# Kernel tuning notes

Measured on AMD Instinct MI355X. Metric: run time of the kernel, lower is better.

The kernel has to match this reference:

```python
import jax, jax.numpy as jnp
import numpy as np

IMG = 840.0
MIN_SIZES = [[16.0, 32.0], [64.0, 128.0], [256.0, 512.0]]
STEPS = [8, 16, 32]
THRESH = 0.35      # neg_overlap / matching threshold used by this repo's MultiBoxLoss
NEG_POS = 7
LOC_WEIGHT = 2.0
VAR0, VAR1 = 0.1, 0.2


def _make_priors():
    out = []
    for ms, step in zip(MIN_SIZES, STEPS):
        f = int(np.ceil(IMG / step))
        jj, ii = np.meshgrid(np.arange(f), np.arange(f))  # j: cols (x), i: rows (y)
        cx = (jj + 0.5) * step / IMG
        cy = (ii + 0.5) * step / IMG
        for m in ms:
            s = np.full_like(cx, m / IMG)
            out.append(np.stack([cx, cy, s, s], axis=-1).reshape(-1, 4))
    return np.concatenate(out, axis=0).astype(np.float32)  # [29126, 4] (cx, cy, w, h)


def setup_inputs() -> dict:
    key = jax.random.key(0)
    k1, k2, k3, k4 = jax.random.split(key, 4)
    B, G = 64, 24
    priors = jnp.asarray(_make_priors())            # [P, 4]
    P = priors.shape[0]
    loc_data = 0.1 * jax.random.normal(k1, (B, P, 4), dtype=jnp.float32)
    conf_data = jax.random.normal(k2, (B, P, 2), dtype=jnp.float32)
    cxy = jax.random.uniform(k3, (B, G, 2), minval=0.2, maxval=0.8)
    wh = jax.random.uniform(k4, (B, G, 2), minval=0.05, maxval=0.3)
    gt_boxes = jnp.clip(jnp.concatenate([cxy - wh / 2, cxy + wh / 2], axis=-1), 1e-3, 1.0)
    gt_labels = jnp.ones((B, G), dtype=jnp.int32)   # single foreground class (num_classes=2)
    return {"loc_data": loc_data, "conf_data": conf_data, "gt_boxes": gt_boxes,
            "gt_labels": gt_labels, "priors": priors}


def _multibox_loss(loc_data, conf_data, gt_boxes, gt_labels, priors):
    B, P, _ = loc_data.shape
    G = gt_boxes.shape[1]
    # priors in point form for IoU
    pr_pt = jnp.concatenate([priors[:, :2] - priors[:, 2:] / 2,
                             priors[:, :2] + priors[:, 2:] / 2], axis=1)  # [P,4]
    area_p = (pr_pt[:, 2] - pr_pt[:, 0]) * (pr_pt[:, 3] - pr_pt[:, 1])

    def match_one(truths, labels):
        # IoU [G, P]
        lt = jnp.maximum(truths[:, None, :2], pr_pt[None, :, :2])
        rb = jnp.minimum(truths[:, None, 2:], pr_pt[None, :, 2:])
        wh = jnp.clip(rb - lt, 0.0)
        inter = wh[..., 0] * wh[..., 1]
        area_t = (truths[:, 2] - truths[:, 0]) * (truths[:, 3] - truths[:, 1])
        iou = inter / (area_t[:, None] + area_p[None, :] - inter)
        best_prior_idx = jnp.argmax(iou, axis=1)          # [G]
        bto = jnp.max(iou, axis=0)                        # [P] best truth overlap
        bti = jnp.argmax(iou, axis=0)                     # [P] best truth idx
        bto = bto.at[best_prior_idx].set(2.0)             # ensure each gt keeps its best prior
        bti = bti.at[best_prior_idx].set(jnp.arange(G))
        matched = truths[bti]                             # [P,4]
        conf = jnp.where(bto < THRESH, 0, labels[bti])    # [P]
        # encode (SSD style, variances 0.1/0.2)
        g_cxcy = ((matched[:, :2] + matched[:, 2:]) / 2 - priors[:, :2]) / (VAR0 * priors[:, 2:])
        g_wh = jnp.log((matched[:, 2:] - matched[:, :2]) / priors[:, 2:]) / VAR1
        return jnp.concatenate([g_cxcy, g_wh], axis=1), conf

    loc_t, conf_t = jax.vmap(match_one)(gt_boxes, gt_labels)  # [B,P,4], [B,P]
    pos = conf_t > 0                                          # [B,P]

    # localization: smooth L1 over positives
    diff = jnp.abs(loc_data - loc_t)
    sl1 = jnp.where(diff < 1.0, 0.5 * diff * diff, diff - 0.5)
    loss_l = jnp.sum(sl1 * pos[..., None].astype(loc_data.dtype))

    # per-prior CE = logsumexp - logit[target]
    lse = jax.nn.logsumexp(conf_data, axis=-1)                               # [B,P]
    gold = jnp.take_along_axis(conf_data, conf_t[..., None], axis=-1)[..., 0]
    ce_all = lse - gold                                                      # [B,P]

    # hard negative mining: rank background-class loss of negatives
    mine = jnp.where(pos, 0.0, ce_all)
    rank = jnp.argsort(jnp.argsort(-mine, axis=1), axis=1)
    num_pos = jnp.sum(pos, axis=1, keepdims=True)                            # [B,1]
    num_neg = jnp.minimum(NEG_POS * num_pos, P - 1)
    neg = rank < num_neg

    mask = pos | neg
    loss_c = jnp.sum(jnp.where(mask, ce_all, 0.0))

    N = jnp.maximum(jnp.sum(pos).astype(loc_data.dtype), 1.0)
    return loss_l / N, loss_c / N


def reference(loc_data, conf_data, gt_boxes, gt_labels, priors):
    loss_l, loss_c = _multibox_loss(loc_data, conf_data, gt_boxes, gt_labels, priors)
    return LOC_WEIGHT * loss_l + loss_c
```

## Files before the change

### kernel.cpp

```cpp
#include <hip/hip_runtime.h>

static constexpr int B_ = 64;
static constexpr int P_ = 29126;
static constexpr int G_ = 24;
static constexpr float THRESH_ = 0.35f;
static constexpr int NEGPOS_ = 7;
static constexpr int PBL_ = (P_ + 1023) / 1024;
static constexpr int PPAD_ = PBL_ * 1024;
static constexpr int NBL_ = PBL_ * B_;
static constexpr int WPB_ = 912;
static constexpr int CCS_ = 32;

__device__ const float LAD_[16] = {
    0.5f,    0.5901f, 0.6964f, 0.8220f, 0.9701f, 1.1450f, 1.3514f, 1.5950f,
    1.8825f, 2.2218f, 2.6223f, 3.0950f, 3.6529f, 4.3113f, 5.0885f, 6.0057f };

static constexpr size_t ZBYTES_ =
    (size_t)B_*WPB_*4 + (size_t)B_*CCS_*4 + 16;
static constexpr int ZVEC_ = (int)((ZBYTES_ + 15) / 16);

__global__ __launch_bounds__(256) void k_zero(ulonglong2* __restrict__ dst)
{
    const int i = blockIdx.x*256 + threadIdx.x;
    if (i < ZVEC_) dst[i] = make_ulonglong2(0ull, 0ull);
}

__global__ __launch_bounds__(256) void k_sparse(
    const float4* __restrict__ gt4,
    const float4* __restrict__ priors4,
    unsigned* __restrict__ matchw,
    unsigned long long* __restrict__ bp_pack)
{
    const int g = blockIdx.x;
    const int b = blockIdx.y;
    const int bg = b*G_ + g;
    const int tid = threadIdx.x;

    const float4 t = gt4[bg];
    const float area_t = (t.z - t.x) * (t.w - t.y);

    float bv = -1.0f; int bq = 0;

#pragma unroll
    for (int r = 0; r < 6; ++r) {
        const int   f    = (r < 2) ? 105 : (r < 4) ? 53 : 27;
        const float sc   = (r < 2) ? 105.0f : (r < 4) ? 52.5f : 26.25f;
        const int   base = (r == 0) ? 0 : (r == 1) ? 11025 : (r == 2) ? 22050
                         : (r == 3) ? 24859 : (r == 4) ? 27668 : 28397;
        const float hw   = ((r == 0) ? 16.0f : (r == 1) ? 32.0f : (r == 2) ? 64.0f
                         : (r == 3) ? 128.0f : (r == 4) ? 256.0f : 512.0f)
                           * (0.5f / 840.0f);

        const int j0 = max(0,     (int)floorf((t.x - hw)*sc - 0.5f) - 1);
        const int j1 = min(f - 1, (int)ceilf ((t.z + hw)*sc - 0.5f) + 1);
        const int i0 = max(0,     (int)floorf((t.y - hw)*sc - 0.5f) - 1);
        const int i1 = min(f - 1, (int)ceilf ((t.w + hw)*sc - 0.5f) + 1);
        const int W = j1 - j0 + 1;
        const int n = W * (i1 - i0 + 1);

        for (int c = tid; c < n; c += 256) {
            const int ii = c / W;
            const int jj = c - ii*W;
            const int p = base + (i0 + ii)*f + (j0 + jj);
            const float4 pr = priors4[p];
            const float hx = pr.z * 0.5f, hy = pr.w * 0.5f;
            const float px0 = pr.x - hx, py0 = pr.y - hy;
            const float px1 = pr.x + hx, py1 = pr.y + hy;
            const float area_p = (px1 - px0) * (py1 - py0);
            const float lx = fmaxf(t.x, px0), ly = fmaxf(t.y, py0);
            const float rx = fminf(t.z, px1), ry = fminf(t.w, py1);
            const float iw = fmaxf(rx - lx, 0.0f), ih = fmaxf(ry - ly, 0.0f);
            const float inter = iw * ih;
            const float iou = __fdividef(inter, (area_t + area_p) - inter);

            if (iou >= THRESH_)
                atomicOr(&matchw[b*WPB_ + (p >> 5)], 1u << (p & 31));
            if (iou > bv) { bv = iou; bq = p; }
        }
    }

    const int lane = tid & 63, wave = tid >> 6;
    for (int m = 32; m; m >>= 1) {
        const float ov = __shfl_xor(bv, m, 64);
        const int   oq = __shfl_xor(bq, m, 64);
        if (ov > bv || (ov == bv && oq < bq)) { bv = ov; bq = oq; }
    }
    __shared__ float swv[4];
    __shared__ int   swq[4];
    if (lane == 0) { swv[wave] = bv; swq[wave] = bq; }
    __syncthreads();
    if (tid == 0) {
        float v = swv[0]; int q = swq[0];
#pragma unroll
        for (int w = 1; w < 4; ++w)
            if (swv[w] > v || (swv[w] == v && swq[w] < q)) { v = swv[w]; q = swq[w]; }
        bp_pack[bg] = (v >= 0.0f)
            ? (((unsigned long long)__float_as_uint(v) << 32)
               | (unsigned long long)(~(unsigned int)q))
            : 0ull;
    }
}

__global__ __launch_bounds__(256) void k_loss(
    const float4* __restrict__ loc4,
    const float2* __restrict__ conf2,
    const float4* __restrict__ gt4,
    const int* __restrict__ labels,
    const float4* __restrict__ priors4,
    const unsigned* __restrict__ matchw,
    const unsigned long long* __restrict__ bp_pack,
    float* __restrict__ mine,
    float* __restrict__ pl, float* __restrict__ pc, int* __restrict__ pp,
    unsigned int* __restrict__ pcnt)
{
    const int b = blockIdx.y;
    const int tid = threadIdx.x;
    const int lane = tid & 63, wave = tid >> 6;
    const int pbase = blockIdx.x*1024;

    __shared__ float4 sgt[G_];
    __shared__ float  sarea[G_];
    __shared__ int    slab[G_];
    __shared__ int    sovr[1024];
    if (tid < G_) {
        const float4 t = gt4[b*G_ + tid];
        sgt[tid] = t;
        sarea[tid] = (t.z - t.x) * (t.w - t.y);
        slab[tid] = labels[b*G_ + tid];
    }
    for (int i = tid; i < 1024; i += 256) sovr[i] = -1;
    __syncthreads();
    if (tid < G_) {
        const unsigned long long pk = bp_pack[b*G_ + tid];
        const int q = (int)(~(unsigned int)(pk & 0xFFFFFFFFull)) - pbase;
        if (q >= 0 && q < 1024) atomicMax(&sovr[q], tid);
    }
    __syncthreads();

    const int p0 = pbase + tid*4;
    float lL = 0.0f, pce = 0.0f; int np = 0;
    unsigned q0 = 0, q1 = 0, q2 = 0, q3 = 0, q4 = 0, q5 = 0, q6 = 0, q7 = 0;
    float m4[4] = {0.0f, 0.0f, 0.0f, 0.0f};

    const bool anyValid = (p0 < P_);
    if (anyValid) {
        const unsigned mw = (matchw[b*WPB_ + (p0 >> 5)] >> (p0 & 31)) & 0xFu;
        const int4 ov4 = *(const int4*)&sovr[tid*4];
        const int og[4] = { ov4.x, ov4.y, ov4.z, ov4.w };
        const bool full = (p0 + 3 < P_);

        float cf[8];
        if (full) {
            const float4* c4 = (const float4*)conf2;
            const size_t base2 = ((size_t)b*P_ + p0) >> 1;
            const float4 ca = c4[base2];
            const float4 cb = c4[base2 + 1];
            cf[0]=ca.x; cf[1]=ca.y; cf[2]=ca.z; cf[3]=ca.w;
            cf[4]=cb.x; cf[5]=cb.y; cf[6]=cb.z; cf[7]=cb.w;
        } else {
            for (int c = 0; c < 4; ++c) {
                if (p0 + c < P_) {
                    const float2 x = conf2[(size_t)b*P_ + p0 + c];
                    cf[2*c] = x.x; cf[2*c+1] = x.y;
                } else { cf[2*c] = 0.0f; cf[2*c+1] = 0.0f; }
            }
        }

        float ce4[4];
#pragma unroll
        for (int c = 0; c < 4; ++c)
            ce4[c] = __logf(1.0f + __expf(cf[2*c+1] - cf[2*c]));

        unsigned spec = 0;
#pragma unroll
        for (int c = 0; c < 4; ++c)
            if (og[c] >= 0 || ((mw >> c) & 1u)) spec |= (1u << c);

#pragma unroll
        for (int c = 0; c < 4; ++c)
            if (p0 + c < P_) m4[c] = ce4[c];

        if (__any(spec != 0u)) {
#pragma unroll
            for (int c = 0; c < 4; ++c) {
                const int p = p0 + c;
                if (((spec >> c) & 1u) && p < P_) {
                    int cc = 0, g = 0;
                    if (og[c] >= 0) { g = og[c]; cc = slab[g]; }
                    else {
                        const float4 pr = priors4[p];
                        const float hx = pr.z * 0.5f, hy = pr.w * 0.5f;
                        const float px0 = pr.x - hx, py0 = pr.y - hy;
                        const float px1 = pr.x + hx, py1 = pr.y + hy;
                        const float area_p = (px1 - px0) * (py1 - py0);
                        float best = -1.0f;
#pragma unroll
                        for (int gg = 0; gg < G_; ++gg) {
                            const float4 t = sgt[gg];
                            const float lx = fmaxf(t.x, px0), ly = fmaxf(t.y, py0);
                            const float rx = fminf(t.z, px1), ry = fminf(t.w, py1);
                            const float iw = fmaxf(rx - lx, 0.0f), ih = fmaxf(ry - ly, 0.0f);
                            const float inter = iw * ih;
                            const float iou = __fdividef(inter, (sarea[gg] + area_p) - inter);
                            if (iou > best) { best = iou; g = gg; }
                        }
                        cc = slab[g];
                    }
                    if (cc > 0) {
                        const float ce = __logf(1.0f + __expf(cf[2*c] - cf[2*c+1]));
                        np += 1; pce += ce; m4[c] = 0.0f;
                        const float4 t  = sgt[g];
                        const float4 pr = priors4[p];
                        const float gcx = __fdividef((t.x + t.z)*0.5f - pr.x, 0.1f*pr.z);
                        const float gcy = __fdividef((t.y + t.w)*0.5f - pr.y, 0.1f*pr.w);
                        const float gw  = __logf(__fdividef(t.z - t.x, pr.z)) * 5.0f;
                        const float gh  = __logf(__fdividef(t.w - t.y, pr.w)) * 5.0f;
                        const float4 l = loc4[(size_t)b*P_ + p];
                        const float d0 = fabsf(l.x - gcx);
                        const float d1 = fabsf(l.y - gcy);
                        const float d2 = fabsf(l.z - gw);
                        const float d3 = fabsf(l.w - gh);
                        lL += (d0 < 1.0f) ? 0.5f*d0*d0 : d0 - 0.5f;
                        lL += (d1 < 1.0f) ? 0.5f*d1*d1 : d1 - 0.5f;
                        lL += (d2 < 1.0f) ? 0.5f*d2*d2 : d2 - 0.5f;
                        lL += (d3 < 1.0f) ? 0.5f*d3*d3 : d3 - 0.5f;
                    }
                }
            }
        }

#pragma unroll
        for (int c = 0; c < 4; ++c) {
            if (p0 + c < P_) {
                const float m = m4[c];
                q0 += (unsigned)(m > 0.5f)    + ((unsigned)(m > 0.5901f) << 16);
                q1 += (unsigned)(m > 0.6964f) + ((unsigned)(m > 0.8220f) << 16);
                q2 += (unsigned)(m > 0.9701f) + ((unsigned)(m > 1.1450f) << 16);
                q3 += (unsigned)(m > 1.3514f) + ((unsigned)(m > 1.5950f) << 16);
                q4 += (unsigned)(m > 1.8825f) + ((unsigned)(m > 2.2218f) << 16);
                q5 += (unsigned)(m > 2.6223f) + ((unsigned)(m > 3.0950f) << 16);
                q6 += (unsigned)(m > 3.6529f) + ((unsigned)(m > 4.3113f) << 16);
                q7 += (unsigned)(m > 5.0885f) + ((unsigned)(m > 6.0057f) << 16);
            }
        }

        float* mrow = mine + (size_t)b*PPAD_ + p0;
        if (full) {
            *(float4*)mrow = make_float4(m4[0], m4[1], m4[2], m4[3]);
        } else {
            for (int c = 0; c < 4; ++c)
                if (p0 + c < P_) mrow[c] = m4[c];
        }
    }

    for (int m = 32; m; m >>= 1) {
        lL  += __shfl_xor(lL, m, 64);
        pce += __shfl_xor(pce, m, 64);
        np  += __shfl_xor(np, m, 64);
        q0 += __shfl_xor(q0, m, 64); q1 += __shfl_xor(q1, m, 64);
        q2 += __shfl_xor(q2, m, 64); q3 += __shfl_xor(q3, m, 64);
        q4 += __shfl_xor(q4, m, 64); q5 += __shfl_xor(q5, m, 64);
        q6 += __shfl_xor(q6, m, 64); q7 += __shfl_xor(q7, m, 64);
    }
    __shared__ float swL[4], swC[4];
    __shared__ int   swP[4];
    __shared__ unsigned swu[4][8];
    if (lane == 0) {
        swL[wave] = lL; swC[wave] = pce; swP[wave] = np;
        swu[wave][0] = q0; swu[wave][1] = q1; swu[wave][2] = q2; swu[wave][3] = q3;
        swu[wave][4] = q4; swu[wave][5] = q5; swu[wave][6] = q6; swu[wave][7] = q7;
    }
    __syncthreads();
    const int o = b*PBL_ + blockIdx.x;
    if (tid == 0) {
        pl[o] = swL[0] + swL[1] + swL[2] + swL[3];
        pc[o] = swC[0] + swC[1] + swC[2] + swC[3];
        pp[o] = swP[0] + swP[1] + swP[2] + swP[3];
    }
    if (tid < 8)
        pcnt[o*8 + tid] = swu[0][tid] + swu[1][tid] + swu[2][tid] + swu[3][tid];
}

__device__ inline void bracket_block(
    const unsigned int* __restrict__ pcnt, const int* __restrict__ pp,
    int b, int tid, int4* out, int* np_out)
{
    __shared__ int sred[256];
    sred[tid] = (tid < PBL_) ? pp[b*PBL_ + tid] : 0;
    __syncthreads();
    for (int off = 128; off > 0; off >>= 1) {
        if (tid < off) sred[tid] += sred[tid+off];
        __syncthreads();
    }
    const int np = sred[0];
    int k = NEGPOS_ * np; if (k > P_-1) k = P_-1;

    __shared__ unsigned red[32][8];
    {
        const int i = tid >> 3, j = tid & 7;
        red[i][j] = (i < PBL_) ? pcnt[(b*PBL_ + i)*8 + j] : 0u;
    }
    __syncthreads();
    for (int off = 16; off > 0; off >>= 1) {
        const int i = tid >> 3, j = tid & 7;
        if (i < off) red[i][j] += red[i+off][j];
        __syncthreads();
    }
    __shared__ int C[16];
    if (tid < 8) {
        C[2*tid]   = (int)(red[0][tid] & 0xFFFFu);
        C[2*tid+1] = (int)(red[0][tid] >> 16);
    }
    __shared__ int4 sbr;
    __syncthreads();
    if (tid == 0) {
        int4 s; s.w = 0;
        if (k <= 0) {
            s.x = 0x7F800000; s.y = 0x7F800000; s.z = 0;
        } else {
            int js = -1;
            for (int j = 0; j < 16; ++j) if (C[j] >= k) js = j;
            if (js < 0) {
                s.x = __float_as_int(LAD_[0]);
                s.y = __float_as_int(-1.0f);
                s.z = k - C[0];
            } else if (js == 15) {
                s.x = 0x7F800000;
                s.y = __float_as_int(LAD_[15]);
                s.z = k;
            } else {
                s.x = __float_as_int(LAD_[js+1]);
                s.y = __float_as_int(LAD_[js]);
                s.z = k - C[js+1];
            }
        }
        sbr = s;
    }
    __syncthreads();
    *out = sbr;
    *np_out = np;
}

__global__ __launch_bounds__(256) void k_collect(
    const float* __restrict__ mine,
    const unsigned int* __restrict__ pcnt, const int* __restrict__ pp,
    unsigned int* __restrict__ cand, int* __restrict__ candCount,
    float* __restrict__ pcol)
{
    const int b = blockIdx.y;
    const int tid = threadIdx.x;
    const int lane = tid & 63;

    int4 se; int np_dummy;
    bracket_block(pcnt, pp, b, tid, &se, &np_dummy);
    const float hi = __int_as_float(se.x);
    const float lo = __int_as_float(se.y);

    __shared__ unsigned int sbuf[1024];
    __shared__ int scnt;
    __shared__ int gbase;
    if (tid == 0) scnt = 0;
    __syncthreads();

    const int p0 = blockIdx.x*1024 + tid*4;
    float v4[4] = {-1.0f, -1.0f, -1.0f, -1.0f};
    if (p0 + 3 < P_) {
        const float4 v = *(const float4*)(mine + (size_t)b*PPAD_ + p0);
        v4[0] = v.x; v4[1] = v.y; v4[2] = v.z; v4[3] = v.w;
    } else if (p0 < P_) {
        for (int c = 0; c < 4; ++c)
            if (p0 + c < P_) v4[c] = mine[(size_t)b*PPAD_ + p0 + c];
    }

    float sum = 0.0f;
#pragma unroll
    for (int c = 0; c < 4; ++c) {
        const float v = v4[c];
        bool isCand = false;
        if (v > hi) sum += v;
        else isCand = (v > lo);
        const unsigned long long mask = __ballot(isCand);
        const int wcnt = __popcll(mask);
        int wbase = 0;
        if (lane == 0 && wcnt) wbase = atomicAdd(&scnt, wcnt);
        wbase = __shfl(wbase, 0, 64);
        if (isCand) {
            const int before = __popcll(mask & ((1ull << lane) - 1ull));
            sbuf[wbase + before] = __float_as_uint(v);
        }
    }
    __syncthreads();
    const int tot = scnt;
    if (tid == 0) gbase = tot ? atomicAdd(&candCount[b*CCS_], tot) : 0;
    __syncthreads();
    for (int i = tid; i < tot; i += 256)
        cand[(size_t)b*P_ + gbase + i] = sbuf[i];

    __shared__ float sf2[256];
    sf2[tid] = sum;
    __syncthreads();
    for (int off = 128; off > 0; off >>= 1) {
        if (tid < off) sf2[tid] += sf2[tid+off];
        __syncthreads();
    }
    if (tid == 0) pcol[b*PBL_ + blockIdx.x] = sf2[0];
}

__global__ __launch_bounds__(256) void k_sel2fin(
    const unsigned int* __restrict__ cand, const int* __restrict__ candCount,
    const unsigned int* __restrict__ pcnt, const int* __restrict__ pp,
    const float* __restrict__ pl, const float* __restrict__ pc,
    const float* __restrict__ pcol,
    float4* __restrict__ outb, unsigned int* __restrict__ ticket,
    float* __restrict__ out)
{
    const int b = blockIdx.x;
    const int tid = threadIdx.x;

    int4 se; int np;
    bracket_block(pcnt, pp, b, tid, &se, &np);
    const int kk = se.z;

    __shared__ float rA[256], rB[256], rC2[256];
    rA[tid]  = (tid < PBL_) ? pl[b*PBL_ + tid] : 0.0f;
    rB[tid]  = (tid < PBL_) ? pc[b*PBL_ + tid] : 0.0f;
    rC2[tid] = (tid < PBL_) ? pcol[b*PBL_ + tid] : 0.0f;
    __syncthreads();
    for (int off = 128; off > 0; off >>= 1) {
        if (tid < off) {
            rA[tid] += rA[tid+off];
            rB[tid] += rB[tid+off];
            rC2[tid] += rC2[tid+off];
        }
        __syncthreads();
    }
    const float sumL = rA[0], sumC = rB[0], sumhi = rC2[0];
    __syncthreads();

    float ctopv = sumhi;
    const int nc = candCount[b*CCS_];
    if (kk > 0 && nc > 0) {
        const unsigned int* row = cand + (size_t)b * P_;
        __shared__ unsigned int hist[256];
        __shared__ unsigned int sc0[256], sc1[256];
        __shared__ unsigned int sh_prefix;
        __shared__ int sh_kk;

        unsigned int prefix = 0; int kk2 = kk;
        for (int pass = 3; pass >= 0; --pass) {
            hist[tid] = 0;
            __syncthreads();
            const unsigned int highmask =
                (pass == 3) ? 0u : (0xFFFFFFFFu << ((pass+1)*8));
            for (int i = tid; i < nc; i += 256) {
                const unsigned int u = row[i];
                if ((u & highmask) == (prefix & highmask))
                    atomicAdd(&hist[(u >> (pass*8)) & 255u], 1u);
            }
            __syncthreads();
            sc0[tid] = hist[255 - tid];
            __syncthreads();
            unsigned int* src = sc0; unsigned int* dst = sc1;
            for (int off = 1; off < 256; off <<= 1) {
                unsigned int v = src[tid];
                if (tid >= off) v += src[tid - off];
                dst[tid] = v;
                __syncthreads();
                unsigned int* t2 = src; src = dst; dst = t2;
            }
            {
                const int bin = 255 - tid;
                const int cum = (int)src[tid];
                const int cumPrev = (tid == 0) ? 0 : (int)src[tid-1];
                if (cum >= kk2 && cumPrev < kk2) {
                    sh_prefix = prefix | ((unsigned int)bin << (pass*8));
                    sh_kk = kk2 - cumPrev;
                }
            }
            __syncthreads();
            prefix = sh_prefix; kk2 = sh_kk;
            __syncthreads();
        }

        const float T = __uint_as_float(prefix);
        float sum = 0.0f; int cnt = 0;
        for (int i = tid; i < nc; i += 256) {
            const unsigned int u = row[i];
            if (u > prefix) { sum += __uint_as_float(u); ++cnt; }
        }
        __shared__ float sf[256];
        __shared__ int   sci[256];
        sf[tid] = sum; sci[tid] = cnt;
        __syncthreads();
        for (int off = 128; off > 0; off >>= 1) {
            if (tid < off) { sf[tid] += sf[tid+off]; sci[tid] += sci[tid+off]; }
            __syncthreads();
        }
        ctopv = sumhi + sf[0] + (float)(kk - sci[0]) * T;
    }

    __shared__ int sdone;
    if (tid == 0) {
        outb[b] = make_float4(sumL, sumC, (float)np, ctopv);
        __threadfence();
        sdone = (int)atomicAdd(ticket, 1u);
    }
    __syncthreads();
    if (sdone == B_ - 1) {
        __threadfence();
        float L = 0.0f, C = 0.0f, Pn = 0.0f, T = 0.0f;
        if (tid < B_) {
            const float4 v = outb[tid];
            L = v.x; C = v.y; Pn = v.z; T = v.w;
        }
        for (int m = 32; m; m >>= 1) {
            L += __shfl_xor(L, m, 64);
            C += __shfl_xor(C, m, 64);
            Pn += __shfl_xor(Pn, m, 64);
            T += __shfl_xor(T, m, 64);
        }
        if (tid == 0)
            out[0] = (2.0f*L + C + T) / fmaxf(Pn, 1.0f);
    }
}

extern "C" void kernel_launch(void* const* d_in, const int* in_sizes, int n_in,
                              void* d_out, int out_size, void* d_ws, size_t ws_size,
                              hipStream_t stream)
{
    const float* loc    = (const float*)d_in[0];
    const float* conf   = (const float*)d_in[1];
    const float* gt     = (const float*)d_in[2];
    const int*   labels = (const int*)d_in[3];
    const float* priors = (const float*)d_in[4];
    float* out = (float*)d_out;

    char* ws = (char*)d_ws;
    size_t off = 0;
    unsigned* matchw = (unsigned*)(ws + off);        off += (size_t)B_*WPB_*4;
    int* candCount = (int*)(ws + off);               off += (size_t)B_*CCS_*4;
    unsigned int* ticket = (unsigned int*)(ws + off); off += 16;
    off = (off + 255) & ~255ull;
    unsigned long long* bp_pack =
        (unsigned long long*)(ws + off);             off += (size_t)B_*G_*8;
    float* mine = (float*)(ws + off);                off += (size_t)B_*PPAD_*4;
    float* pl   = (float*)(ws + off);                off += (size_t)NBL_*4;
    float* pc   = (float*)(ws + off);                off += (size_t)NBL_*4;
    int*   pp   = (int*)(ws + off);                  off += (size_t)NBL_*4;
    float* pcol = (float*)(ws + off);                off += (size_t)NBL_*4;
    unsigned int* pcnt = (unsigned int*)(ws + off);  off += (size_t)NBL_*8*4;
    unsigned int* cand = (unsigned int*)(ws + off);  off += (size_t)B_*P_*4;
    float4* outb = (float4*)(ws + off);              off += (size_t)B_*16;

    k_zero<<<dim3((ZVEC_ + 255)/256), dim3(256), 0, stream>>>((ulonglong2*)ws);
    k_sparse<<<dim3(G_, B_), dim3(256), 0, stream>>>(
        (const float4*)gt, (const float4*)priors, matchw, bp_pack);
    k_loss<<<dim3(PBL_, B_), dim3(256), 0, stream>>>(
        (const float4*)loc, (const float2*)conf, (const float4*)gt, labels,
        (const float4*)priors, matchw, bp_pack, mine, pl, pc, pp, pcnt);
    k_collect<<<dim3(PBL_, B_), dim3(256), 0, stream>>>(
        mine, pcnt, pp, cand, candCount, pcol);
    k_sel2fin<<<dim3(B_), dim3(256), 0, stream>>>(
        cand, candCount, pcnt, pp, pl, pc, pcol, outb, ticket, out);
}
```

Measured before the change: 75.33 us.

## Drop mine buffer; recompute logit difference in collect with positive bitmask

The per-prior mined-loss array is no longer written by the loss kernel or read back by the collect kernel. The collect kernel instead rereads conf, rebuilds the logit difference z, and masks positives using a new per-batch bitmask that the loss kernel sets with atomicOr. Histogram thresholds and candidate selection now work on z, which is monotone with the softplus loss, so softplus is only evaluated for the selected values. This removes a B*P float write and read, at the cost of a second conf read, atomics on the bitmask, and zeroing a larger region.

```diff
diff --git a/kernel.cpp b/kernel.cpp
--- a/kernel.cpp
+++ b/kernel.cpp
@@ -6,18 +6,26 @@
 static constexpr float THRESH_ = 0.35f;
 static constexpr int NEGPOS_ = 7;
 static constexpr int PBL_ = (P_ + 1023) / 1024;
-static constexpr int PPAD_ = PBL_ * 1024;
 static constexpr int NBL_ = PBL_ * B_;
 static constexpr int WPB_ = 912;
 static constexpr int CCS_ = 32;
 
 __device__ const float LAD_[16] = {
-    0.5f,    0.5901f, 0.6964f, 0.8220f, 0.9701f, 1.1450f, 1.3514f, 1.5950f,
-    1.8825f, 2.2218f, 2.6223f, 3.0950f, 3.6529f, 4.3113f, 5.0885f, 6.0057f };
+    -0.5f, -0.2f, 0.0f, 0.2f, 0.4f, 0.6f, 0.8f, 1.0f,
+     1.2f,  1.4f, 1.6f, 1.8f, 2.1f, 2.4f, 2.8f, 3.3f };
 
 static constexpr size_t ZBYTES_ =
-    (size_t)B_*WPB_*4 + (size_t)B_*CCS_*4 + 16;
+    (size_t)B_*WPB_*4*2 + (size_t)B_*CCS_*4 + 16;
 static constexpr int ZVEC_ = (int)((ZBYTES_ + 15) / 16);
+
+__device__ inline unsigned zmap(float z) {
+    const unsigned f = __float_as_uint(z);
+    return (f & 0x80000000u) ? ~f : (f | 0x80000000u);
+}
+__device__ inline float zunmap(unsigned u) {
+    const unsigned f = (u & 0x80000000u) ? (u & 0x7FFFFFFFu) : ~u;
+    return __uint_as_float(f);
+}
 
 __global__ __launch_bounds__(256) void k_zero(ulonglong2* __restrict__ dst)
 {
@@ -101,15 +109,15 @@
     }
 }
 
-__global__ __launch_bounds__(256) void k_loss(
+__global__ __launch_bounds__(256) void k_count(
     const float4* __restrict__ loc4,
     const float2* __restrict__ conf2,
     const float4* __restrict__ gt4,
     const int* __restrict__ labels,
     const float4* __restrict__ priors4,
     const unsigned* __restrict__ matchw,
+    unsigned* __restrict__ posw,
     const unsigned long long* __restrict__ bp_pack,
-    float* __restrict__ mine,
     float* __restrict__ pl, float* __restrict__ pc, int* __restrict__ pp,
     unsigned int* __restrict__ pcnt)
 {
@@ -140,10 +148,8 @@
     const int p0 = pbase + tid*4;
     float lL = 0.0f, pce = 0.0f; int np = 0;
     unsigned q0 = 0, q1 = 0, q2 = 0, q3 = 0, q4 = 0, q5 = 0, q6 = 0, q7 = 0;
-    float m4[4] = {0.0f, 0.0f, 0.0f, 0.0f};
-
-    const bool anyValid = (p0 < P_);
-    if (anyValid) {
+
+    if (p0 < P_) {
         const unsigned mw = (matchw[b*WPB_ + (p0 >> 5)] >> (p0 & 31)) & 0xFu;
         const int4 ov4 = *(const int4*)&sovr[tid*4];
         const int og[4] = { ov4.x, ov4.y, ov4.z, ov4.w };
@@ -162,25 +168,23 @@
                 if (p0 + c < P_) {
                     const float2 x = conf2[(size_t)b*P_ + p0 + c];
                     cf[2*c] = x.x; cf[2*c+1] = x.y;
-                } else { cf[2*c] = 0.0f; cf[2*c+1] = 0.0f; }
-            }
-        }
-
-        float ce4[4];
+                } else { cf[2*c] = -1e30f; cf[2*c+1] = -1e30f; }
+            }
+        }
+
+        float z4[4];
 #pragma unroll
         for (int c = 0; c < 4; ++c)
-            ce4[c] = __logf(1.0f + __expf(cf[2*c+1] - cf[2*c]));
+            z4[c] = (p0 + c < P_) ? (cf[2*c+1] - cf[2*c])
+                                  : -__int_as_float(0x7F800000);
 
         unsigned spec = 0;
 #pragma unroll
         for (int c = 0; c < 4; ++c)
             if (og[c] >= 0 || ((mw >> c) & 1u)) spec |= (1u << c);
 
-#pragma unroll
-        for (int c = 0; c < 4; ++c)
-            if (p0 + c < P_) m4[c] = ce4[c];
-
         if (__any(spec != 0u)) {
+            unsigned posbits = 0;
 #pragma unroll
             for (int c = 0; c < 4; ++c) {
                 const int p = p0 + c;
@@ -208,7 +212,9 @@
                     }
                     if (cc > 0) {
                         const float ce = __logf(1.0f + __expf(cf[2*c] - cf[2*c+1]));
-                        np += 1; pce += ce; m4[c] = 0.0f;
+                        np += 1; pce += ce;
+                        z4[c] = -__int_as_float(0x7F800000);
+                        posbits |= (1u << (p0 & 31)) << c;
                         const float4 t  = sgt[g];
                         const float4 pr = priors4[p];
                         const float gcx = __fdividef((t.x + t.z)*0.5f - pr.x, 0.1f*pr.z);
@@ -227,29 +233,20 @@
                     }
                 }
             }
+            if (posbits) atomicOr(&posw[b*WPB_ + (p0 >> 5)], posbits);
         }
 
 #pragma unroll
         for (int c = 0; c < 4; ++c) {
-            if (p0 + c < P_) {
-                const float m = m4[c];
-                q0 += (unsigned)(m > 0.5f)    + ((unsigned)(m > 0.5901f) << 16);
-                q1 += (unsigned)(m > 0.6964f) + ((unsigned)(m > 0.8220f) << 16);
-                q2 += (unsigned)(m > 0.9701f) + ((unsigned)(m > 1.1450f) << 16);
-                q3 += (unsigned)(m > 1.3514f) + ((unsigned)(m > 1.5950f) << 16);
-                q4 += (unsigned)(m > 1.8825f) + ((unsigned)(m > 2.2218f) << 16);
-                q5 += (unsigned)(m > 2.6223f) + ((unsigned)(m > 3.0950f) << 16);
-                q6 += (unsigned)(m > 3.6529f) + ((unsigned)(m > 4.3113f) << 16);
-                q7 += (unsigned)(m > 5.0885f) + ((unsigned)(m > 6.0057f) << 16);
-            }
-        }
-
-        float* mrow = mine + (size_t)b*PPAD_ + p0;
-        if (full) {
-            *(float4*)mrow = make_float4(m4[0], m4[1], m4[2], m4[3]);
-        } else {
-            for (int c = 0; c < 4; ++c)
-                if (p0 + c < P_) mrow[c] = m4[c];
+            const float z = z4[c];
+            q0 += (unsigned)(z > -0.5f) + ((unsigned)(z > -0.2f) << 16);
+            q1 += (unsigned)(z >  0.0f) + ((unsigned)(z >  0.2f) << 16);
+            q2 += (unsigned)(z >  0.4f) + ((unsigned)(z >  0.6f) << 16);
+            q3 += (unsigned)(z >  0.8f) + ((unsigned)(z >  1.0f) << 16);
+            q4 += (unsigned)(z >  1.2f) + ((unsigned)(z >  1.4f) << 16);
+            q5 += (unsigned)(z >  1.6f) + ((unsigned)(z >  1.8f) << 16);
+            q6 += (unsigned)(z >  2.1f) + ((unsigned)(z >  2.4f) << 16);
+            q7 += (unsigned)(z >  2.8f) + ((unsigned)(z >  3.3f) << 16);
         }
     }
 
@@ -322,7 +319,7 @@
             for (int j = 0; j < 16; ++j) if (C[j] >= k) js = j;
             if (js < 0) {
                 s.x = __float_as_int(LAD_[0]);
-                s.y = __float_as_int(-1.0f);
+                s.y = (int)0xFF800000;
                 s.z = k - C[0];
             } else if (js == 15) {
                 s.x = 0x7F800000;
@@ -342,7 +339,8 @@
 }
 
 __global__ __launch_bounds__(256) void k_collect(
-    const float* __restrict__ mine,
+    const float2* __restrict__ conf2,
+    const unsigned* __restrict__ posw,
     const unsigned int* __restrict__ pcnt, const int* __restrict__ pp,
     unsigned int* __restrict__ cand, int* __restrict__ candCount,
     float* __restrict__ pcol)
@@ -363,22 +361,37 @@
     __syncthreads();
 
     const int p0 = blockIdx.x*1024 + tid*4;
-    float v4[4] = {-1.0f, -1.0f, -1.0f, -1.0f};
-    if (p0 + 3 < P_) {
-        const float4 v = *(const float4*)(mine + (size_t)b*PPAD_ + p0);
-        v4[0] = v.x; v4[1] = v.y; v4[2] = v.z; v4[3] = v.w;
-    } else if (p0 < P_) {
+    float z4[4] = { -__int_as_float(0x7F800000), -__int_as_float(0x7F800000),
+                    -__int_as_float(0x7F800000), -__int_as_float(0x7F800000) };
+    if (p0 < P_) {
+        const unsigned pw = (posw[b*WPB_ + (p0 >> 5)] >> (p0 & 31)) & 0xFu;
+        if (p0 + 3 < P_) {
+            const float4* c4 = (const float4*)conf2;
+            const size_t base2 = ((size_t)b*P_ + p0) >> 1;
+            const float4 ca = c4[base2];
+            const float4 cb = c4[base2 + 1];
+            z4[0] = ca.y - ca.x; z4[1] = ca.w - ca.z;
+            z4[2] = cb.y - cb.x; z4[3] = cb.w - cb.z;
+        } else {
+            for (int c = 0; c < 4; ++c) {
+                if (p0 + c < P_) {
+                    const float2 x = conf2[(size_t)b*P_ + p0 + c];
+                    z4[c] = x.y - x.x;
+                }
+            }
+        }
+#pragma unroll
         for (int c = 0; c < 4; ++c)
-            if (p0 + c < P_) v4[c] = mine[(size_t)b*PPAD_ + p0 + c];
+            if ((pw >> c) & 1u) z4[c] = -__int_as_float(0x7F800000);
     }
 
     float sum = 0.0f;
 #pragma unroll
     for (int c = 0; c < 4; ++c) {
-        const float v = v4[c];
+        const float z = z4[c];
         bool isCand = false;
-        if (v > hi) sum += v;
-        else isCand = (v > lo);
+        if (z > hi) sum += __logf(1.0f + __expf(z));
+        else isCand = (z > lo);
         const unsigned long long mask = __ballot(isCand);
         const int wcnt = __popcll(mask);
         int wbase = 0;
@@ -386,7 +399,7 @@
         wbase = __shfl(wbase, 0, 64);
         if (isCand) {
             const int before = __popcll(mask & ((1ull << lane) - 1ull));
-            sbuf[wbase + before] = __float_as_uint(v);
+            sbuf[wbase + before] = zmap(z);
         }
     }
     __syncthreads();
@@ -482,11 +495,15 @@
             __syncthreads();
         }
 
-        const float T = __uint_as_float(prefix);
+        const float zT = zunmap(prefix);
+        const float T = __logf(1.0f + __expf(zT));
         float sum = 0.0f; int cnt = 0;
         for (int i = tid; i < nc; i += 256) {
             const unsigned int u = row[i];
-            if (u > prefix) { sum += __uint_as_float(u); ++cnt; }
+            if (u > prefix) {
+                sum += __logf(1.0f + __expf(zunmap(u)));
+                ++cnt;
+            }
         }
         __shared__ float sf[256];
         __shared__ int   sci[256];
@@ -538,12 +555,12 @@
     char* ws = (char*)d_ws;
     size_t off = 0;
     unsigned* matchw = (unsigned*)(ws + off);        off += (size_t)B_*WPB_*4;
+    unsigned* posw   = (unsigned*)(ws + off);        off += (size_t)B_*WPB_*4;
     int* candCount = (int*)(ws + off);               off += (size_t)B_*CCS_*4;
     unsigned int* ticket = (unsigned int*)(ws + off); off += 16;
     off = (off + 255) & ~255ull;
     unsigned long long* bp_pack =
         (unsigned long long*)(ws + off);             off += (size_t)B_*G_*8;
-    float* mine = (float*)(ws + off);                off += (size_t)B_*PPAD_*4;
     float* pl   = (float*)(ws + off);                off += (size_t)NBL_*4;
     float* pc   = (float*)(ws + off);                off += (size_t)NBL_*4;
     int*   pp   = (int*)(ws + off);                  off += (size_t)NBL_*4;
@@ -555,11 +572,11 @@
     k_zero<<<dim3((ZVEC_ + 255)/256), dim3(256), 0, stream>>>((ulonglong2*)ws);
     k_sparse<<<dim3(G_, B_), dim3(256), 0, stream>>>(
         (const float4*)gt, (const float4*)priors, matchw, bp_pack);
-    k_loss<<<dim3(PBL_, B_), dim3(256), 0, stream>>>(
+    k_count<<<dim3(PBL_, B_), dim3(256), 0, stream>>>(
         (const float4*)loc, (const float2*)conf, (const float4*)gt, labels,
-        (const float4*)priors, matchw, bp_pack, mine, pl, pc, pp, pcnt);
+        (const float4*)priors, matchw, posw, bp_pack, pl, pc, pp, pcnt);
     k_collect<<<dim3(PBL_, B_), dim3(256), 0, stream>>>(
-        mine, pcnt, pp, cand, candCount, pcol);
+        (const float2*)conf, posw, pcnt, pp, cand, candCount, pcol);
     k_sel2fin<<<dim3(B_), dim3(256), 0, stream>>>(
         cand, candCount, pcnt, pp, pl, pc, pcol, outb, ticket, out);
 }
```

After: 73.14 us (median of 2 runs). -2.9%, faster.
